# Performance work log

Hardware: AMD Instinct MI355X
Metric: run time of the kernel (lower is better)

The kernel has to match this reference:

```python
import jax, jax.numpy as jnp
import numpy as np

D = 1024  # decoder_hidden_dim


def setup_inputs() -> dict:
    key = jax.random.key(0)
    k1, k2, k3, k4 = jax.random.split(key, 4)
    b, s, d = 32, 2048, D
    decoder_hidden = jax.random.normal(k1, (b, d), dtype=jnp.float32)
    encoder_all_hidden = jax.random.normal(k2, (b, s, d), dtype=jnp.float32)
    # torch nn.Linear(2d, d, bias=False): weight shape (d, 2d)
    W_a = jax.random.normal(k3, (d, 2 * d), dtype=jnp.float32) * (1.0 / np.sqrt(2 * d))
    # torch nn.Linear(d, 1, bias=False): weight shape (1, d) -> store as (d,)
    v = jax.random.normal(k4, (d,), dtype=jnp.float32) * (1.0 / np.sqrt(d))
    return {"decoder_hidden": decoder_hidden, "encoder_all_hidden": encoder_all_hidden,
            "W_a": W_a, "v": v}


def reference(decoder_hidden, encoder_all_hidden, W_a, v):
    d = W_a.shape[0]
    # Split W_a so the (b, s, 2d) concat is never materialized:
    # cat([dec, enc]) @ W_a^T == dec @ Wd^T + enc @ We^T
    Wd = W_a[:, :d]   # acts on decoder part
    We = W_a[:, d:]   # acts on encoder part
    dec_proj = jnp.einsum('bd,ed->be', decoder_hidden, Wd)          # (b, d)
    enc_proj = jnp.einsum('bsd,ed->bse', encoder_all_hidden, We)    # (b, s, d)
    h = jnp.tanh(dec_proj[:, None, :] + enc_proj)                   # (b, s, d)
    scores = jnp.einsum('bse,e->bs', h, v)                          # (b, s)
    alpha = jax.nn.softmax(scores, axis=1)
    return alpha
```

## Files before the change

kernel.cpp:

```cpp
#include <hip/hip_runtime.h>
#include <hip/hip_bf16.h>
#include <stdint.h>


typedef __bf16 bf16x8 __attribute__((ext_vector_type(8)));
typedef __bf16 bf16x2 __attribute__((ext_vector_type(2)));
typedef float floatx4 __attribute__((ext_vector_type(4)));
typedef unsigned short ushort_t;

#define M_TOT 65536
#define D_DIM 1024
#define WA_LD 2048
#define S_DIM 2048

#define VMCNT4 asm volatile("s_waitcnt vmcnt(4)" ::: "memory")
#define VMCNT0 asm volatile("s_waitcnt vmcnt(0)" ::: "memory")
#define BAR    __builtin_amdgcn_s_barrier()
#define SCHED0 __builtin_amdgcn_sched_barrier(0)

__device__ __forceinline__ unsigned int pack2(float a, float b) {
#if __has_builtin(__builtin_amdgcn_cvt_pk_bf16_f32)
    bf16x2 p = __builtin_amdgcn_cvt_pk_bf16_f32(a, b);
    return __builtin_bit_cast(unsigned int, p);
#else
    unsigned int ua = __float_as_uint(a), ub = __float_as_uint(b);
    ua += 0x7fffu + ((ua >> 16) & 1u);
    ub += 0x7fffu + ((ub >> 16) & 1u);
    return __builtin_amdgcn_perm(ub, ua, 0x07060302);
#endif
}

__device__ __forceinline__ void gl16(const ushort_t* g, ushort_t* l) {
    __builtin_amdgcn_global_load_lds(
        (const __attribute__((address_space(1))) unsigned int*)g,
        (__attribute__((address_space(3))) unsigned int*)l,
        16, 0, 0);
}

__global__ __launch_bounds__(256) void convertW_kernel(
    const float* __restrict__ Wa, ushort_t* __restrict__ Web)
{
    const int e = blockIdx.x;
    const int k = threadIdx.x * 4;
    float4 wv = *(const float4*)(Wa + (size_t)e * WA_LD + D_DIM + k);
    uint2 pk = { pack2(wv.x, wv.y), pack2(wv.z, wv.w) };
    *(uint2*)(Web + (size_t)e * D_DIM + k) = pk;
}

__global__ __launch_bounds__(256) void convert_enc_kernel(
    const float* __restrict__ in, ushort_t* __restrict__ out)
{
    size_t i = ((size_t)blockIdx.x * 256 + threadIdx.x) * 8;
    const size_t stride = (size_t)4096 * 256 * 8;
    for (int it = 0; it < 8; ++it, i += stride) {
        float4 a = *(const float4*)(in + i);
        float4 b = *(const float4*)(in + i + 4);
        uint4 pk = { pack2(a.x, a.y), pack2(a.z, a.w), pack2(b.x, b.y), pack2(b.z, b.w) };
        *(uint4*)(out + i) = pk;
    }
}

__global__ __launch_bounds__(256) void decproj_kernel(
    const float* __restrict__ dec,
    const float* __restrict__ Wa,
    float* __restrict__ dp)
{
    const int b    = blockIdx.y;
    const int wave = threadIdx.x >> 6;
    const int lane = threadIdx.x & 63;
    const int e    = blockIdx.x * 4 + wave;

    __shared__ float s_d[1024];
    for (int t = threadIdx.x; t < 1024; t += 256)
        s_d[t] = dec[b * 1024 + t];
    __syncthreads();

    const float* wrow = Wa + (size_t)e * WA_LD;
    float sum = 0.f;
    #pragma unroll
    for (int k0 = 0; k0 < 1024; k0 += 256) {
        float4 w = *(const float4*)(wrow + k0 + lane * 4);
        float4 d = *(const float4*)(&s_d[k0 + lane * 4]);
        sum += w.x * d.x + w.y * d.y + w.z * d.z + w.w * d.w;
    }
    #pragma unroll
    for (int msk = 1; msk < 64; msk <<= 1)
        sum += __shfl_xor(sum, msk, 64);
    if (lane == 0)
        dp[b * 1024 + e] = sum;
}

__device__ __forceinline__ void stage_step(
    const ushort_t* Ag, const ushort_t* Bg, int k0,
    ushort_t* a0, ushort_t* a1, ushort_t* b0, ushort_t* b1)
{
    gl16(Ag + k0,              a0);
    gl16(Ag + k0 + 64 * D_DIM, a1);
    gl16(Bg + k0,              b0);
    gl16(Bg + k0 + 64 * D_DIM, b1);
}

__device__ __forceinline__ void compute_step(
    const ushort_t* Asb, const ushort_t* Bsb,
    const int* offA, const int* offB, floatx4 acc[4][4])
{
    bf16x8 af[4], bfr[4];
    #pragma unroll
    for (int i = 0; i < 4; ++i) af[i]  = *(const bf16x8*)(Asb + offA[i]);
    #pragma unroll
    for (int j = 0; j < 4; ++j) bfr[j] = *(const bf16x8*)(Bsb + offB[j]);
    #pragma unroll
    for (int i = 0; i < 4; ++i)
        #pragma unroll
        for (int j = 0; j < 4; ++j)
            acc[i][j] = __builtin_amdgcn_mfma_f32_16x16x32_bf16(af[i], bfr[j], acc[i][j], 0, 0, 0);
}

__global__ __launch_bounds__(256) void gemm_bf16_kernel(
    const ushort_t* __restrict__ A,
    const ushort_t* __restrict__ Bw,
    const float* __restrict__ v,
    const float* __restrict__ dp,
    float* __restrict__ partial)
{
    __shared__ ushort_t As[2][128 * 32];
    __shared__ ushort_t Bs[2][128 * 32];
    __shared__ float s_dec[128], s_v[128], s_score[128];

    const int tid  = threadIdx.x;
    const int lane = tid & 63;
    const int w    = tid >> 6;
    const int wm   = w >> 1;
    const int wn   = w & 1;
    const int r16  = lane & 15;
    const int q    = lane >> 4;

    const int flat    = blockIdx.y * 8 + blockIdx.x;
    const int n_block = (flat >> 3) & 7;
    const int m_block = (flat & 7) | ((flat >> 6) << 3);
    const int b_idx   = m_block >> 4;

    if (tid < 128) {
        s_dec[tid] = dp[b_idx * 1024 + n_block * 128 + tid];
        s_v[tid]   = v[n_block * 128 + tid];
    }
    __syncthreads();

    const int sr = (w << 4) + (lane >> 2);
    const int fS = (sr & 3) ^ ((sr >> 2) & 1);
    const int sg = ((lane & 3) ^ fS) << 3;
    const ushort_t* Ag = A  + (size_t)(m_block * 128 + sr) * D_DIM + sg;
    const ushort_t* Bg = Bw + (size_t)(n_block * 128 + sr) * D_DIM + sg;
    const int wbase0 = (w << 4) * 32;
    const int wbase1 = (64 + (w << 4)) * 32;

    const int fR = (r16 & 3) ^ ((r16 >> 2) & 1);
    const int sl = (q ^ fR) << 3;
    int offA[4], offB[4];
    #pragma unroll
    for (int i = 0; i < 4; ++i) {
        offA[i] = (wm * 64 + i * 16 + r16) * 32 + sl;
        offB[i] = (wn * 64 + i * 16 + r16) * 32 + sl;
    }

    floatx4 acc[4][4] = {};

    stage_step(Ag, Bg, 0, &As[0][wbase0], &As[0][wbase1], &Bs[0][wbase0], &Bs[0][wbase1]);

    for (int t = 0; t < 30; t += 2) {
        stage_step(Ag, Bg, (t + 1) * 32, &As[1][wbase0], &As[1][wbase1], &Bs[1][wbase0], &Bs[1][wbase1]);
        VMCNT4; BAR; SCHED0;
        compute_step(As[0], Bs[0], offA, offB, acc);
        SCHED0; BAR;
        stage_step(Ag, Bg, (t + 2) * 32, &As[0][wbase0], &As[0][wbase1], &Bs[0][wbase0], &Bs[0][wbase1]);
        VMCNT4; BAR; SCHED0;
        compute_step(As[1], Bs[1], offA, offB, acc);
        SCHED0; BAR;
    }
    stage_step(Ag, Bg, 31 * 32, &As[1][wbase0], &As[1][wbase1], &Bs[1][wbase0], &Bs[1][wbase1]);
    VMCNT4; BAR; SCHED0;
    compute_step(As[0], Bs[0], offA, offB, acc);
    SCHED0; BAR;
    VMCNT0; BAR; SCHED0;
    compute_step(As[1], Bs[1], offA, offB, acc);

    float p[4][4] = {};
    #pragma unroll
    for (int j = 0; j < 4; ++j) {
        const int nl = wn * 64 + j * 16 + r16;
        const float dd = s_dec[nl];
        const float vv = s_v[nl];
        #pragma unroll
        for (int i = 0; i < 4; ++i) {
            #pragma unroll
            for (int r = 0; r < 4; ++r) {
                float x = acc[i][j][r] + dd;
                if (!(x > -8.f)) x = -8.f;
                if (x > 8.f)     x = 8.f;
                float e2 = __expf(2.f * x);
                float h  = 1.f - 2.f * __builtin_amdgcn_rcpf(e2 + 1.f);
                p[i][r] += h * vv;
            }
        }
    }
    #pragma unroll
    for (int msk = 1; msk < 16; msk <<= 1) {
        #pragma unroll
        for (int i = 0; i < 4; ++i)
            #pragma unroll
            for (int r = 0; r < 4; ++r)
                p[i][r] += __shfl_xor(p[i][r], msk, 64);
    }
    __syncthreads();
    if (wn == 0 && r16 == 0) {
        #pragma unroll
        for (int i = 0; i < 4; ++i)
            #pragma unroll
            for (int r = 0; r < 4; ++r)
                s_score[wm * 64 + i * 16 + q * 4 + r] = p[i][r];
    }
    __syncthreads();
    if (wn == 1 && r16 == 0) {
        #pragma unroll
        for (int i = 0; i < 4; ++i)
            #pragma unroll
            for (int r = 0; r < 4; ++r)
                s_score[wm * 64 + i * 16 + q * 4 + r] += p[i][r];
    }
    __syncthreads();
    if (tid < 128)
        partial[(size_t)n_block * M_TOT + m_block * 128 + tid] = s_score[tid];
}

__global__ __launch_bounds__(256) void fused_gemm_fp32_kernel(
    const float* __restrict__ enc,
    const float* __restrict__ Wa,
    const float* __restrict__ v,
    const float* __restrict__ dp,
    float* __restrict__ partial)
{
    __shared__ unsigned short As[128 * 32];
    __shared__ unsigned short Bs[128 * 32];
    __shared__ float s_dec[128];
    __shared__ float s_v[128];
    __shared__ float s_score[128];

    const int tid  = threadIdx.x;
    const int lane = tid & 63;
    const int wave = tid >> 6;
    const int wm   = wave >> 1;
    const int wn   = wave & 1;

    const int flat    = blockIdx.y * 8 + blockIdx.x;
    const int n_block = (flat >> 3) & 7;
    const int m_block = (flat & 7) | ((flat >> 6) << 3);
    const int b_idx   = m_block >> 4;

    if (tid < 128) {
        s_dec[tid] = dp[b_idx * 1024 + n_block * 128 + tid];
        s_v[tid]   = v[n_block * 128 + tid];
    }

    const int r0  = tid >> 2;
    const int kk  = (tid & 3) * 8;
    const int r16 = lane & 15;
    const int q   = lane >> 4;

    const float* A_base = enc + (size_t)m_block * 128 * D_DIM;
    const float* B_base = Wa + (size_t)n_block * 128 * WA_LD + D_DIM;

    floatx4 acc[4][4] = {};

    for (int k0 = 0; k0 < 1024; k0 += 32) {
        float4 a0l = *(const float4*)(A_base + (size_t)r0        * D_DIM + k0 + kk);
        float4 a0h = *(const float4*)(A_base + (size_t)r0        * D_DIM + k0 + kk + 4);
        float4 a1l = *(const float4*)(A_base + (size_t)(r0 + 64) * D_DIM + k0 + kk);
        float4 a1h = *(const float4*)(A_base + (size_t)(r0 + 64) * D_DIM + k0 + kk + 4);
        float4 b0l = *(const float4*)(B_base + (size_t)r0        * WA_LD + k0 + kk);
        float4 b0h = *(const float4*)(B_base + (size_t)r0        * WA_LD + k0 + kk + 4);
        float4 b1l = *(const float4*)(B_base + (size_t)(r0 + 64) * WA_LD + k0 + kk);
        float4 b1h = *(const float4*)(B_base + (size_t)(r0 + 64) * WA_LD + k0 + kk + 4);
        uint4 pa0 = { pack2(a0l.x, a0l.y), pack2(a0l.z, a0l.w), pack2(a0h.x, a0h.y), pack2(a0h.z, a0h.w) };
        uint4 pa1 = { pack2(a1l.x, a1l.y), pack2(a1l.z, a1l.w), pack2(a1h.x, a1h.y), pack2(a1h.z, a1h.w) };
        uint4 pb0 = { pack2(b0l.x, b0l.y), pack2(b0l.z, b0l.w), pack2(b0h.x, b0h.y), pack2(b0h.z, b0h.w) };
        uint4 pb1 = { pack2(b1l.x, b1l.y), pack2(b1l.z, b1l.w), pack2(b1h.x, b1h.y), pack2(b1h.z, b1h.w) };
        __syncthreads();
        *(uint4*)&As[r0        * 32 + kk] = pa0;
        *(uint4*)&As[(r0 + 64) * 32 + kk] = pa1;
        *(uint4*)&Bs[r0        * 32 + kk] = pb0;
        *(uint4*)&Bs[(r0 + 64) * 32 + kk] = pb1;
        __syncthreads();

        bf16x8 af[4], bfr[4];
        #pragma unroll
        for (int i = 0; i < 4; ++i)
            af[i] = *(const bf16x8*)&As[(wm * 64 + i * 16 + r16) * 32 + q * 8];
        #pragma unroll
        for (int j = 0; j < 4; ++j)
            bfr[j] = *(const bf16x8*)&Bs[(wn * 64 + j * 16 + r16) * 32 + q * 8];
        #pragma unroll
        for (int i = 0; i < 4; ++i)
            #pragma unroll
            for (int j = 0; j < 4; ++j)
                acc[i][j] = __builtin_amdgcn_mfma_f32_16x16x32_bf16(af[i], bfr[j], acc[i][j], 0, 0, 0);
    }

    float p[4][4] = {};
    #pragma unroll
    for (int j = 0; j < 4; ++j) {
        const int nl = wn * 64 + j * 16 + r16;
        const float dd = s_dec[nl];
        const float vv = s_v[nl];
        #pragma unroll
        for (int i = 0; i < 4; ++i) {
            #pragma unroll
            for (int r = 0; r < 4; ++r) {
                float x = acc[i][j][r] + dd;
                if (!(x > -8.f)) x = -8.f;
                if (x > 8.f)     x = 8.f;
                float e2 = __expf(2.f * x);
                float h  = 1.f - 2.f * __builtin_amdgcn_rcpf(e2 + 1.f);
                p[i][r] += h * vv;
            }
        }
    }
    #pragma unroll
    for (int msk = 1; msk < 16; msk <<= 1) {
        #pragma unroll
        for (int i = 0; i < 4; ++i)
            #pragma unroll
            for (int r = 0; r < 4; ++r)
                p[i][r] += __shfl_xor(p[i][r], msk, 64);
    }
    __syncthreads();
    if (wn == 0 && r16 == 0) {
        #pragma unroll
        for (int i = 0; i < 4; ++i)
            #pragma unroll
            for (int r = 0; r < 4; ++r)
                s_score[wm * 64 + i * 16 + q * 4 + r] = p[i][r];
    }
    __syncthreads();
    if (wn == 1 && r16 == 0) {
        #pragma unroll
        for (int i = 0; i < 4; ++i)
            #pragma unroll
            for (int r = 0; r < 4; ++r)
                s_score[wm * 64 + i * 16 + q * 4 + r] += p[i][r];
    }
    __syncthreads();
    if (tid < 128)
        partial[(size_t)n_block * M_TOT + m_block * 128 + tid] = s_score[tid];
}

__global__ __launch_bounds__(1024) void softmax_kernel(
    const float* __restrict__ partial,
    float* __restrict__ out)
{
    const int b = blockIdx.x;
    const int tid = threadIdx.x;
    const int wv = tid >> 6;
    __shared__ float wred[16];

    float sc[2];
    float mx = -1e30f;
    #pragma unroll
    for (int ii = 0; ii < 2; ++ii) {
        const int s = tid + ii * 1024;
        float sum = 0.f;
        #pragma unroll
        for (int pp = 0; pp < 8; ++pp)
            sum += partial[(size_t)pp * M_TOT + b * S_DIM + s];
        sc[ii] = sum;
        mx = fmaxf(mx, sum);
    }
    #pragma unroll
    for (int msk = 1; msk < 64; msk <<= 1) mx = fmaxf(mx, __shfl_xor(mx, msk, 64));
    if ((tid & 63) == 0) wred[wv] = mx;
    __syncthreads();
    #pragma unroll
    for (int k = 0; k < 16; ++k) mx = fmaxf(mx, wred[k]);
    __syncthreads();

    float ex[2];
    float tot = 0.f;
    #pragma unroll
    for (int ii = 0; ii < 2; ++ii) { ex[ii] = __expf(sc[ii] - mx); tot += ex[ii]; }
    #pragma unroll
    for (int msk = 1; msk < 64; msk <<= 1) tot += __shfl_xor(tot, msk, 64);
    if ((tid & 63) == 0) wred[wv] = tot;
    __syncthreads();
    tot = 0.f;
    #pragma unroll
    for (int k = 0; k < 16; ++k) tot += wred[k];
    const float inv = 1.f / tot;
    #pragma unroll
    for (int ii = 0; ii < 2; ++ii)
        out[b * S_DIM + tid + ii * 1024] = ex[ii] * inv;
}

extern "C" void kernel_launch(void* const* d_in, const int* in_sizes, int n_in,
                              void* d_out, int out_size, void* d_ws, size_t ws_size,
                              hipStream_t stream) {
    (void)in_sizes; (void)n_in; (void)out_size;
    const float* dec = (const float*)d_in[0];
    const float* enc = (const float*)d_in[1];
    const float* Wa  = (const float*)d_in[2];
    const float* v   = (const float*)d_in[3];
    float* out = (float*)d_out;

    float* dp      = (float*)d_ws;
    float* partial = dp + 32 * 1024;

    const size_t NEED = (size_t)(32 * 1024 + 8 * 65536) * 4
                      + (size_t)67108864 * 2
                      + (size_t)1048576 * 2;

    if (ws_size >= NEED) {
        ushort_t* encb = (ushort_t*)(partial + 8 * 65536);
        ushort_t* Web  = encb + 67108864;
        convertW_kernel<<<dim3(1024), 256, 0, stream>>>(Wa, Web);
        convert_enc_kernel<<<dim3(4096), 256, 0, stream>>>(enc, encb);
        decproj_kernel<<<dim3(256, 32), 256, 0, stream>>>(dec, Wa, dp);
        gemm_bf16_kernel<<<dim3(8, 512), 256, 0, stream>>>(encb, Web, v, dp, partial);
    } else {
        decproj_kernel<<<dim3(256, 32), 256, 0, stream>>>(dec, Wa, dp);
        fused_gemm_fp32_kernel<<<dim3(8, 512), 256, 0, stream>>>(enc, Wa, v, dp, partial);
    }
    softmax_kernel<<<32, 1024, 0, stream>>>(partial, out);
}
```

Measured before the change: 574.3 us.

## Enlarge bf16 GEMM tile to 256x128 with triple-buffered A and 512 threads

The bf16 GEMM now uses 512-thread blocks over 256x128 output tiles with a K step of 64. A is triple-buffered and B double-buffered in LDS, with loads for later steps issued between the split half-phases and MFMA sections run at raised wave priority. The larger tile raises data reuse per LDS byte and halves the grid, while the added LDS use and registers may lower occupancy. The decoder projection kernel now loads every batch row into shared memory and reuses each W row across all 32 batches, cutting repeated reads of W_a.

```diff
diff --git a/kernel.cpp b/kernel.cpp
--- a/kernel.cpp
+++ b/kernel.cpp
@@ -13,8 +13,12 @@
 #define WA_LD 2048
 #define S_DIM 2048
 
+#define A_TILE 16384
+#define B_TILE 8192
+
 #define VMCNT4 asm volatile("s_waitcnt vmcnt(4)" ::: "memory")
 #define VMCNT0 asm volatile("s_waitcnt vmcnt(0)" ::: "memory")
+#define LGKM0  asm volatile("s_waitcnt lgkmcnt(0)" ::: "memory")
 #define BAR    __builtin_amdgcn_s_barrier()
 #define SCHED0 __builtin_amdgcn_sched_barrier(0)
 
@@ -65,133 +69,169 @@
     const float* __restrict__ Wa,
     float* __restrict__ dp)
 {
-    const int b    = blockIdx.y;
-    const int wave = threadIdx.x >> 6;
-    const int lane = threadIdx.x & 63;
+    __shared__ float s_d[32 * 1024];
+    const int tid  = threadIdx.x;
+    const int wave = tid >> 6;
+    const int lane = tid & 63;
     const int e    = blockIdx.x * 4 + wave;
 
-    __shared__ float s_d[1024];
-    for (int t = threadIdx.x; t < 1024; t += 256)
-        s_d[t] = dec[b * 1024 + t];
+    for (int idx = tid; idx < 8192; idx += 256)
+        *(float4*)&s_d[idx * 4] = *(const float4*)&dec[idx * 4];
     __syncthreads();
 
     const float* wrow = Wa + (size_t)e * WA_LD;
-    float sum = 0.f;
-    #pragma unroll
-    for (int k0 = 0; k0 < 1024; k0 += 256) {
-        float4 w = *(const float4*)(wrow + k0 + lane * 4);
-        float4 d = *(const float4*)(&s_d[k0 + lane * 4]);
-        sum += w.x * d.x + w.y * d.y + w.z * d.z + w.w * d.w;
-    }
-    #pragma unroll
-    for (int msk = 1; msk < 64; msk <<= 1)
-        sum += __shfl_xor(sum, msk, 64);
-    if (lane == 0)
-        dp[b * 1024 + e] = sum;
-}
-
-__device__ __forceinline__ void stage_step(
-    const ushort_t* Ag, const ushort_t* Bg, int k0,
-    ushort_t* a0, ushort_t* a1, ushort_t* b0, ushort_t* b1)
-{
-    gl16(Ag + k0,              a0);
-    gl16(Ag + k0 + 64 * D_DIM, a1);
-    gl16(Bg + k0,              b0);
-    gl16(Bg + k0 + 64 * D_DIM, b1);
-}
-
-__device__ __forceinline__ void compute_step(
-    const ushort_t* Asb, const ushort_t* Bsb,
-    const int* offA, const int* offB, floatx4 acc[4][4])
-{
-    bf16x8 af[4], bfr[4];
-    #pragma unroll
-    for (int i = 0; i < 4; ++i) af[i]  = *(const bf16x8*)(Asb + offA[i]);
-    #pragma unroll
-    for (int j = 0; j < 4; ++j) bfr[j] = *(const bf16x8*)(Bsb + offB[j]);
+    float4 wv[4];
     #pragma unroll
     for (int i = 0; i < 4; ++i)
-        #pragma unroll
-        for (int j = 0; j < 4; ++j)
-            acc[i][j] = __builtin_amdgcn_mfma_f32_16x16x32_bf16(af[i], bfr[j], acc[i][j], 0, 0, 0);
-}
-
-__global__ __launch_bounds__(256) void gemm_bf16_kernel(
+        wv[i] = *(const float4*)(wrow + i * 256 + lane * 4);
+
+    for (int b = 0; b < 32; ++b) {
+        float sum = 0.f;
+        #pragma unroll
+        for (int i = 0; i < 4; ++i) {
+            float4 d = *(const float4*)&s_d[b * 1024 + i * 256 + lane * 4];
+            sum += wv[i].x * d.x + wv[i].y * d.y + wv[i].z * d.z + wv[i].w * d.w;
+        }
+        #pragma unroll
+        for (int msk = 1; msk < 64; msk <<= 1)
+            sum += __shfl_xor(sum, msk, 64);
+        if (lane == 0)
+            dp[b * 1024 + e] = sum;
+    }
+}
+
+__global__ __launch_bounds__(512) void gemm_bf16_kernel(
     const ushort_t* __restrict__ A,
     const ushort_t* __restrict__ Bw,
     const float* __restrict__ v,
     const float* __restrict__ dp,
     float* __restrict__ partial)
 {
-    __shared__ ushort_t As[2][128 * 32];
-    __shared__ ushort_t Bs[2][128 * 32];
-    __shared__ float s_dec[128], s_v[128], s_score[128];
+    __shared__ ushort_t Asm[3 * A_TILE];
+    __shared__ ushort_t Bsm[2 * B_TILE];
+    __shared__ float s_dec[128], s_v[128];
+    __shared__ float s_sc[4][256];
 
     const int tid  = threadIdx.x;
     const int lane = tid & 63;
     const int w    = tid >> 6;
-    const int wm   = w >> 1;
-    const int wn   = w & 1;
+    const int wm   = w >> 2;
+    const int wn   = w & 3;
     const int r16  = lane & 15;
     const int q    = lane >> 4;
 
     const int flat    = blockIdx.y * 8 + blockIdx.x;
-    const int n_block = (flat >> 3) & 7;
-    const int m_block = (flat & 7) | ((flat >> 6) << 3);
-    const int b_idx   = m_block >> 4;
+    const int logical = (flat & 7) * 256 + (flat >> 3);
+    const int n_block = logical & 7;
+    const int m_block = logical >> 3;
+    const int b_idx   = m_block >> 3;
+    const int m_base  = m_block * 256;
+    const int n_base  = n_block * 128;
 
     if (tid < 128) {
-        s_dec[tid] = dp[b_idx * 1024 + n_block * 128 + tid];
-        s_v[tid]   = v[n_block * 128 + tid];
-    }
-    __syncthreads();
-
-    const int sr = (w << 4) + (lane >> 2);
-    const int fS = (sr & 3) ^ ((sr >> 2) & 1);
-    const int sg = ((lane & 3) ^ fS) << 3;
-    const ushort_t* Ag = A  + (size_t)(m_block * 128 + sr) * D_DIM + sg;
-    const ushort_t* Bg = Bw + (size_t)(n_block * 128 + sr) * D_DIM + sg;
-    const int wbase0 = (w << 4) * 32;
-    const int wbase1 = (64 + (w << 4)) * 32;
-
-    const int fR = (r16 & 3) ^ ((r16 >> 2) & 1);
-    const int sl = (q ^ fR) << 3;
-    int offA[4], offB[4];
-    #pragma unroll
-    for (int i = 0; i < 4; ++i) {
-        offA[i] = (wm * 64 + i * 16 + r16) * 32 + sl;
-        offB[i] = (wn * 64 + i * 16 + r16) * 32 + sl;
-    }
-
-    floatx4 acc[4][4] = {};
-
-    stage_step(Ag, Bg, 0, &As[0][wbase0], &As[0][wbase1], &Bs[0][wbase0], &Bs[0][wbase1]);
-
-    for (int t = 0; t < 30; t += 2) {
-        stage_step(Ag, Bg, (t + 1) * 32, &As[1][wbase0], &As[1][wbase1], &Bs[1][wbase0], &Bs[1][wbase1]);
-        VMCNT4; BAR; SCHED0;
-        compute_step(As[0], Bs[0], offA, offB, acc);
-        SCHED0; BAR;
-        stage_step(Ag, Bg, (t + 2) * 32, &As[0][wbase0], &As[0][wbase1], &Bs[0][wbase0], &Bs[0][wbase1]);
-        VMCNT4; BAR; SCHED0;
-        compute_step(As[1], Bs[1], offA, offB, acc);
-        SCHED0; BAR;
-    }
-    stage_step(Ag, Bg, 31 * 32, &As[1][wbase0], &As[1][wbase1], &Bs[1][wbase0], &Bs[1][wbase1]);
-    VMCNT4; BAR; SCHED0;
-    compute_step(As[0], Bs[0], offA, offB, acc);
+        s_dec[tid] = dp[b_idx * 1024 + n_base + tid];
+        s_v[tid]   = v[n_base + tid];
+    }
+    __syncthreads();
+
+    const int grow = tid >> 3;
+    const int gcol = (((tid & 7) ^ (grow & 7)) << 3);
+
+    auto stageA = [&](int h, int tsrc) {
+        ushort_t* dst = &Asm[(tsrc % 3) * A_TILE + h * 8192 + w * 512];
+        const ushort_t* src = A + (size_t)(m_base + h * 128 + grow) * D_DIM + tsrc * 64 + gcol;
+        gl16(src, dst);
+        gl16(src + (size_t)64 * D_DIM, dst + 4096);
+    };
+    auto stageB = [&](int tsrc) {
+        ushort_t* dst = &Bsm[(tsrc & 1) * B_TILE + w * 512];
+        const ushort_t* src = Bw + (size_t)(n_base + grow) * D_DIM + tsrc * 64 + gcol;
+        gl16(src, dst);
+        gl16(src + (size_t)64 * D_DIM, dst + 4096);
+    };
+
+    int arow[8], brow[2];
+    #pragma unroll
+    for (int i = 0; i < 8; ++i) arow[i] = (wm * 128 + i * 16 + r16) * 64;
+    #pragma unroll
+    for (int j = 0; j < 2; ++j) brow[j] = (wn * 32 + j * 16 + r16) * 64;
+    const int sl0 = ((q ^ (r16 & 7)) << 3);
+    const int sl1 = sl0 ^ 32;
+
+    floatx4 acc[8][2] = {};
+
+    auto phase = [&](const ushort_t* At, const ushort_t* Bt, int slk) {
+        bf16x8 af[8], bq[2];
+        #pragma unroll
+        for (int i = 0; i < 8; ++i) af[i] = *(const bf16x8*)(At + arow[i] + slk);
+        #pragma unroll
+        for (int j = 0; j < 2; ++j) bq[j] = *(const bf16x8*)(Bt + brow[j] + slk);
+        SCHED0; BAR; LGKM0; SCHED0;
+        __builtin_amdgcn_s_setprio(1);
+        #pragma unroll
+        for (int i = 0; i < 8; ++i)
+            #pragma unroll
+            for (int j = 0; j < 2; ++j)
+                acc[i][j] = __builtin_amdgcn_mfma_f32_16x16x32_bf16(af[i], bq[j], acc[i][j], 0, 0, 0);
+        __builtin_amdgcn_s_setprio(0);
+    };
+
+    stageB(0); stageA(0, 0); stageA(1, 0); stageA(0, 1); stageA(1, 1);
+    VMCNT4;
     SCHED0; BAR;
-    VMCNT0; BAR; SCHED0;
-    compute_step(As[1], Bs[1], offA, offB, acc);
-
-    float p[4][4] = {};
-    #pragma unroll
-    for (int j = 0; j < 4; ++j) {
-        const int nl = wn * 64 + j * 16 + r16;
+
+    for (int t = 0; t < 16; ++t) {
+        const ushort_t* At = &Asm[(t % 3) * A_TILE];
+        const ushort_t* Bt = &Bsm[(t & 1) * B_TILE];
+
+        {
+            bf16x8 af[8], bq[2];
+            #pragma unroll
+            for (int i = 0; i < 8; ++i) af[i] = *(const bf16x8*)(At + arow[i] + sl0);
+            #pragma unroll
+            for (int j = 0; j < 2; ++j) bq[j] = *(const bf16x8*)(Bt + brow[j] + sl0);
+            if (t <= 14) stageB(t + 1);
+            if (t <= 13) stageA(0, t + 2);
+            SCHED0; BAR; LGKM0; SCHED0;
+            __builtin_amdgcn_s_setprio(1);
+            #pragma unroll
+            for (int i = 0; i < 8; ++i)
+                #pragma unroll
+                for (int j = 0; j < 2; ++j)
+                    acc[i][j] = __builtin_amdgcn_mfma_f32_16x16x32_bf16(af[i], bq[j], acc[i][j], 0, 0, 0);
+            __builtin_amdgcn_s_setprio(0);
+            SCHED0; BAR;
+        }
+        {
+            bf16x8 af[8], bq[2];
+            #pragma unroll
+            for (int i = 0; i < 8; ++i) af[i] = *(const bf16x8*)(At + arow[i] + sl1);
+            #pragma unroll
+            for (int j = 0; j < 2; ++j) bq[j] = *(const bf16x8*)(Bt + brow[j] + sl1);
+            if (t <= 13) stageA(1, t + 2);
+            SCHED0; BAR; LGKM0; SCHED0;
+            __builtin_amdgcn_s_setprio(1);
+            #pragma unroll
+            for (int i = 0; i < 8; ++i)
+                #pragma unroll
+                for (int j = 0; j < 2; ++j)
+                    acc[i][j] = __builtin_amdgcn_mfma_f32_16x16x32_bf16(af[i], bq[j], acc[i][j], 0, 0, 0);
+            __builtin_amdgcn_s_setprio(0);
+            if (t <= 13)      { VMCNT4; }
+            else if (t == 14) { VMCNT0; }
+            SCHED0; BAR;
+        }
+    }
+    (void)phase;
+
+    float p[8][4] = {};
+    #pragma unroll
+    for (int j = 0; j < 2; ++j) {
+        const int nl = wn * 32 + j * 16 + r16;
         const float dd = s_dec[nl];
         const float vv = s_v[nl];
         #pragma unroll
-        for (int i = 0; i < 4; ++i) {
+        for (int i = 0; i < 8; ++i) {
             #pragma unroll
             for (int r = 0; r < 4; ++r) {
                 float x = acc[i][j][r] + dd;
@@ -206,30 +246,22 @@
     #pragma unroll
     for (int msk = 1; msk < 16; msk <<= 1) {
         #pragma unroll
-        for (int i = 0; i < 4; ++i)
+        for (int i = 0; i < 8; ++i)
             #pragma unroll
             for (int r = 0; r < 4; ++r)
                 p[i][r] += __shfl_xor(p[i][r], msk, 64);
     }
-    __syncthreads();
-    if (wn == 0 && r16 == 0) {
-        #pragma unroll
-        for (int i = 0; i < 4; ++i)
+    if (r16 == 0) {
+        #pragma unroll
+        for (int i = 0; i < 8; ++i)
             #pragma unroll
             for (int r = 0; r < 4; ++r)
-                s_score[wm * 64 + i * 16 + q * 4 + r] = p[i][r];
-    }
-    __syncthreads();
-    if (wn == 1 && r16 == 0) {
-        #pragma unroll
-        for (int i = 0; i < 4; ++i)
-            #pragma unroll
-            for (int r = 0; r < 4; ++r)
-                s_score[wm * 64 + i * 16 + q * 4 + r] += p[i][r];
-    }
-    __syncthreads();
-    if (tid < 128)
-        partial[(size_t)n_block * M_TOT + m_block * 128 + tid] = s_score[tid];
+                s_sc[wn][wm * 128 + i * 16 + q * 4 + r] = p[i][r];
+    }
+    __syncthreads();
+    if (tid < 256)
+        partial[(size_t)n_block * M_TOT + m_base + tid] =
+            s_sc[0][tid] + s_sc[1][tid] + s_sc[2][tid] + s_sc[3][tid];
 }
 
 __global__ __launch_bounds__(256) void fused_gemm_fp32_kernel(
@@ -421,10 +453,10 @@
         ushort_t* Web  = encb + 67108864;
         convertW_kernel<<<dim3(1024), 256, 0, stream>>>(Wa, Web);
         convert_enc_kernel<<<dim3(4096), 256, 0, stream>>>(enc, encb);
-        decproj_kernel<<<dim3(256, 32), 256, 0, stream>>>(dec, Wa, dp);
-        gemm_bf16_kernel<<<dim3(8, 512), 256, 0, stream>>>(encb, Web, v, dp, partial);
+        decproj_kernel<<<dim3(256), 256, 0, stream>>>(dec, Wa, dp);
+        gemm_bf16_kernel<<<dim3(8, 256), 512, 0, stream>>>(encb, Web, v, dp, partial);
     } else {
-        decproj_kernel<<<dim3(256, 32), 256, 0, stream>>>(dec, Wa, dp);
+        decproj_kernel<<<dim3(256), 256, 0, stream>>>(dec, Wa, dp);
         fused_gemm_fp32_kernel<<<dim3(8, 512), 256, 0, stream>>>(enc, Wa, v, dp, partial);
     }
     softmax_kernel<<<32, 1024, 0, stream>>>(partial, out);
```

Result: slower. 597.7 us (+4.1%).
